# Kernel optimization log

Measured on AMD Instinct MI355X. Metric: run time of the kernel, lower is better.

Reference implementation:

```python
import jax, jax.numpy as jnp
import numpy as np

L_OUT, B, N, C, M, D, T = 4, 4, 1000, 80, 64, 256, 28
CLS_W, L1_W, GIOU_W, MASK_W = 2.0, 5.0, 2.0, 5.0
ALPHA, GAMMA, EPS = 0.25, 2.0, 1e-8
CANDIDATE_K, CENTER_RADIUS, BIG = 10, 2.5, 100000.0


def _areas(b):
    return (b[..., 2] - b[..., 0]) * (b[..., 3] - b[..., 1])


def pairwise_giou(b1, b2):
    # b1 [n,4], b2 [m,4] -> [n,m] generalized IoU (torchvision convention)
    area1, area2 = _areas(b1), _areas(b2)
    lt = jnp.maximum(b1[:, None, :2], b2[None, :, :2])
    rb = jnp.minimum(b1[:, None, 2:], b2[None, :, 2:])
    wh = jnp.clip(rb - lt, 0.0)
    inter = wh[..., 0] * wh[..., 1]
    union = area1[:, None] + area2[None, :] - inter
    iou = inter / union
    lti = jnp.minimum(b1[:, None, :2], b2[None, :, :2])
    rbi = jnp.maximum(b1[:, None, 2:], b2[None, :, 2:])
    whi = jnp.clip(rbi - lti, 0.0)
    areai = whi[..., 0] * whi[..., 1]
    return iou - (areai - union) / areai


def diag_giou(b1, b2):
    # elementwise giou for matched pairs, b1/b2 [n,4] -> [n]
    area1, area2 = _areas(b1), _areas(b2)
    lt = jnp.maximum(b1[:, :2], b2[:, :2])
    rb = jnp.minimum(b1[:, 2:], b2[:, 2:])
    wh = jnp.clip(rb - lt, 0.0)
    inter = wh[:, 0] * wh[:, 1]
    union = area1 + area2 - inter
    iou = inter / union
    lti = jnp.minimum(b1[:, :2], b2[:, :2])
    rbi = jnp.maximum(b1[:, 2:], b2[:, 2:])
    whi = jnp.clip(rbi - lti, 0.0)
    areai = whi[:, 0] * whi[:, 1]
    return iou - (areai - union) / areai


def pairwise_iou(b1, b2, eps=1e-8):
    # mmdet bbox_overlaps, mode='iou'
    area1, area2 = _areas(b1), _areas(b2)
    lt = jnp.maximum(b1[:, None, :2], b2[None, :, :2])
    rb = jnp.minimum(b1[:, None, 2:], b2[None, :, 2:])
    wh = jnp.clip(rb - lt, 0.0)
    inter = wh[..., 0] * wh[..., 1]
    union = jnp.maximum(area1[:, None] + area2[None, :] - inter, eps)
    return inter / union


def simota_match(logits, boxes, gt_cls, gt_boxes, img_size):
    # SimOTA assignment for one image; fixed shapes via masking instead of boolean indexing
    n, c = logits.shape
    m = gt_boxes.shape[0]
    cx = (boxes[:, 0] + boxes[:, 2]) * 0.5
    cy = (boxes[:, 1] + boxes[:, 3]) * 0.5
    w = boxes[:, 2] - boxes[:, 0]
    h = boxes[:, 3] - boxes[:, 1]
    in_gt = ((cx[:, None] > gt_boxes[None, :, 0]) & (cy[:, None] > gt_boxes[None, :, 1])
             & (cx[:, None] < gt_boxes[None, :, 2]) & (cy[:, None] < gt_boxes[None, :, 3]))
    gcx = (gt_boxes[:, 0] + gt_boxes[:, 2]) * 0.5
    gcy = (gt_boxes[:, 1] + gt_boxes[:, 3]) * 0.5
    rx = CENTER_RADIUS * w[:, None]
    ry = CENTER_RADIUS * h[:, None]
    in_ct = ((cx[:, None] > gcx[None, :] - rx) & (cx[:, None] < gcx[None, :] + rx)
             & (cy[:, None] > gcy[None, :] - ry) & (cy[:, None] < gcy[None, :] + ry))
    valid = in_gt.any(1) | in_ct.any(1)
    in_both = in_gt & in_ct
    has_valid = valid.any()
    valid = valid | (~has_valid)          # fallback: all valid when none
    in_both = in_both | (~has_valid)
    # FocalLossCost (mmdet), weight = cls weight
    p = jax.nn.sigmoid(logits)
    neg = -jnp.log(1.0 - p + EPS) * (1.0 - ALPHA) * p ** GAMMA
    pos = -jnp.log(p + EPS) * ALPHA * (1.0 - p) ** GAMMA
    cls_cost = CLS_W * (pos - neg)[:, gt_cls]          # [n,m]
    nb = boxes / img_size
    ngb = gt_boxes / img_size
    l1_cost = L1_W * jnp.abs(nb[:, None, :] - ngb[None, :, :]).sum(-1)
    giou_cost = GIOU_W * (1.0 - pairwise_giou(nb, ngb))
    cost = cls_cost + l1_cost + giou_cost + (~in_both) * BIG
    cost = jnp.where(valid[:, None], cost, 1e15)       # invalid priors never selected
    ious = pairwise_iou(boxes, gt_boxes) * valid[:, None]
    # dynamic_k_matching
    topk_ious, _ = jax.lax.top_k(ious.T, CANDIDATE_K)  # [m,10]
    dyn_k = jnp.maximum(topk_ious.sum(-1).astype(jnp.int32), 1)
    rank = jnp.argsort(jnp.argsort(cost, axis=0), axis=0)
    matching = rank < dyn_k[None, :]                   # [n,m]
    multi = matching.sum(1) > 1
    best = jnp.argmin(cost, axis=1)
    best_oh = best[:, None] == jnp.arange(m)[None, :]
    matching = jnp.where(multi[:, None], best_oh, matching)
    fg = matching.any(1)
    gt_ind = jnp.argmax(matching, axis=1)
    return fg, gt_ind


def per_image_loss(logits, boxes, pfeat, gt_cls, gt_boxes, gt_masks, img_size, w_mask):
    sg = jax.lax.stop_gradient
    fg, gt_ind = simota_match(sg(logits), sg(boxes), gt_cls, sg(gt_boxes), sg(img_size))
    c = logits.shape[1]
    gcls = gt_cls[gt_ind]
    label = jnp.where(fg[:, None], jax.nn.one_hot(gcls, c, dtype=logits.dtype), 0.0)
    # sigmoid focal loss (sum over all n*c logits)
    p = jax.nn.sigmoid(logits)
    ce = -(label * jax.nn.log_sigmoid(logits) + (1.0 - label) * jax.nn.log_sigmoid(-logits))
    p_t = p * label + (1.0 - p) * (1.0 - label)
    alpha_t = ALPHA * label + (1.0 - ALPHA) * (1.0 - label)
    cls_loss = (alpha_t * ce * (1.0 - p_t) ** GAMMA).sum()
    fgf = fg.astype(logits.dtype)
    nb = boxes / img_size
    gb = gt_boxes[gt_ind] / img_size
    l1_loss = (jnp.abs(nb - gb).sum(-1) * fgf).sum()
    giou_loss = ((1.0 - diag_giou(nb, gb)) * fgf).sum()
    # mask head: per-class mask logits from proposal feats; gather only assigned class
    d = pfeat.shape[1]
    tt = T * T
    w_sel = w_mask.reshape(d, c, tt)[:, gcls, :]        # [d,n,tt]
    m_sel = jax.nn.sigmoid(jnp.einsum('nd,dnt->nt', pfeat, w_sel))
    gm = gt_masks.reshape(gt_masks.shape[0], -1)[gt_ind]  # [n,tt]
    inter = (m_sel * gm).sum(-1)
    union = m_sel.sum(-1) + gm.sum(-1) + 1e-8
    mask_loss = ((1.0 - 2.0 * inter / union) * fgf).sum()
    return cls_loss, l1_loss, giou_loss, mask_loss, fgf.sum()


def _forward(pred_logits, pred_boxes, proposal_feat, gt_boxes, gt_masks, image_size, w_mask, gt_classes):
    per = jax.vmap(per_image_loss, in_axes=(0, 0, 0, 0, 0, 0, 0, None))
    total = jnp.zeros(4, dtype=pred_logits.dtype)
    n_out = pred_logits.shape[0]
    for l in range(n_out):   # small fixed loop over output heads
        cl, l1, gl, ml, k = per(pred_logits[l], pred_boxes[l], proposal_feat[l],
                                gt_classes, gt_boxes, gt_masks, image_size, w_mask)
        num_ins = k.sum()
        total = total + jnp.stack([cl.sum(), l1.sum(), gl.sum(), ml.sum()]) / num_ins
    weights = jnp.array([CLS_W, L1_W, GIOU_W, MASK_W], dtype=total.dtype)
    return weights * total / n_out   # [cls, l1, giou, mask] losses


def setup_inputs():
    key = jax.random.key(0)
    ks = jax.random.split(key, 8)

    def rand_boxes(k, shape):
        k1, k2 = jax.random.split(k)
        ctr = jax.random.uniform(k1, shape + (2,), minval=100.0, maxval=700.0)
        wh = jax.random.uniform(k2, shape + (2,), minval=20.0, maxval=300.0)
        return jnp.concatenate([ctr - wh * 0.5, ctr + wh * 0.5], axis=-1)

    pred_logits = jax.random.normal(ks[0], (L_OUT, B, N, C), dtype=jnp.float32)
    pred_boxes = rand_boxes(ks[1], (L_OUT, B, N))
    proposal_feat = 0.1 * jax.random.normal(ks[2], (L_OUT, B, N, D), dtype=jnp.float32)
    gt_boxes = rand_boxes(ks[3], (B, M))
    gt_masks = (jax.random.uniform(ks[4], (B, M, T, T)) > 0.5).astype(jnp.float32)
    image_size = 800.0 * jnp.ones((B,), dtype=jnp.float32)
    w_mask = 0.02 * jax.random.normal(ks[5], (D, C * T * T), dtype=jnp.float32)
    gt_classes = jax.random.randint(ks[6], (B, M), 0, C)
    return {"pred_logits": pred_logits, "pred_boxes": pred_boxes, "proposal_feat": proposal_feat,
            "gt_boxes": gt_boxes, "gt_masks": gt_masks, "image_size": image_size,
            "w_mask": w_mask, "gt_classes": gt_classes}


def reference(pred_logits, pred_boxes, proposal_feat, gt_boxes, gt_masks, image_size, w_mask, gt_classes):
    return _forward(pred_logits, pred_boxes, proposal_feat, gt_boxes, gt_masks, image_size, w_mask, gt_classes)
```

## Files before the change

### kernel.cpp

```cpp
#include <hip/hip_runtime.h>
#include <math.h>
#include <float.h>

#define LOUT 4
#define BATCH 4
#define NP 1000
#define NC 80
#define NM 64
#define ND 256
#define TT 784
#define NIMG (LOUT*BATCH)
#define CWTT (NC*TT)
#define MAXF (NIMG*NP)
#define CH 16
#define TPT 112
#define MAXCH 768

__device__ __forceinline__ float block_reduce_sum(float v, float* red) {
    int tid = threadIdx.x;
    red[tid] = v; __syncthreads();
    for (int s = blockDim.x >> 1; s > 0; s >>= 1) {
        if (tid < s) red[tid] += red[tid + s];
        __syncthreads();
    }
    float r = red[0]; __syncthreads();
    return r;
}

__global__ void __launch_bounds__(256) k_prep(
        const float* __restrict__ logits, const float* __restrict__ boxes,
        const float* __restrict__ gtb, const float* __restrict__ gtm,
        int* __restrict__ valid, unsigned long long* __restrict__ inboth,
        int* __restrict__ hasvalid, float* __restrict__ logT,
        float* __restrict__ negsum, float* __restrict__ gmsum) {
    int blk = blockIdx.x;
    int tid = threadIdx.x;
    __shared__ float red[256];
    __shared__ float tile[32][33];
    if (blk < 256) {
        int bj = blk;
        float s = 0.f;
        for (int t = tid; t < TT; t += 256) s += gtm[(size_t)bj * TT + t];
        float r = block_reduce_sum(s, red);
        if (tid == 0) gmsum[bj] = r;
    } else if (blk < 320) {
        int rel = blk - 256;
        int img = rel >> 2, q = rel & 3, b = img % BATCH;
        float* g = red;
        g[tid] = gtb[b * NM * 4 + tid];
        __syncthreads();
        int i = q * 256 + tid;
        if (i >= NP) return;
        float4 bx = *(const float4*)&boxes[((size_t)img * NP + i) * 4];
        float x0 = bx.x, y0 = bx.y, x1 = bx.z, y1 = bx.w;
        float cx = (x0 + x1) * 0.5f, cy = (y0 + y1) * 0.5f;
        float w = x1 - x0, h = y1 - y0;
        float rx = 2.5f * w, ry = 2.5f * h;
        bool any_gt = false, any_ct = false;
        unsigned long long ib = 0ull;
        for (int j = 0; j < NM; ++j) {
            float gx0 = g[j*4], gy0 = g[j*4+1], gx1 = g[j*4+2], gy1 = g[j*4+3];
            bool igt = (cx > gx0) && (cy > gy0) && (cx < gx1) && (cy < gy1);
            float gcx = (gx0 + gx1) * 0.5f, gcy = (gy0 + gy1) * 0.5f;
            bool ict = (cx > gcx - rx) && (cx < gcx + rx) && (cy > gcy - ry) && (cy < gcy + ry);
            any_gt |= igt; any_ct |= ict;
            if (igt && ict) ib |= (1ull << j);
        }
        bool v = any_gt || any_ct;
        valid[img * NP + i] = v ? 1 : 0;
        inboth[img * NP + i] = ib;
        if (v) atomicOr(&hasvalid[img], 1);
    } else if (blk < 1856) {
        int rel = blk - 320;
        int img = rel / 96; int r2 = rel % 96;
        int i0 = (r2 / 3) * 32, c0 = (r2 % 3) * 32;
        int tx = tid & 31, ty4 = tid >> 5;
        #pragma unroll
        for (int r = 0; r < 4; ++r) {
            int ty = ty4 + r * 8;
            int i = i0 + ty, c = c0 + tx;
            tile[ty][tx] = (i < NP && c < NC) ? logits[((size_t)img * NP + i) * NC + c] : 0.f;
        }
        __syncthreads();
        #pragma unroll
        for (int r = 0; r < 4; ++r) {
            int ty = ty4 + r * 8;
            int c = c0 + ty, i = i0 + tx;
            if (c < NC && i < NP) logT[((size_t)img * NC + c) * NP + i] = tile[tx][ty];
        }
    } else {
        int rel = blk - 1856;
        int img = rel >> 2, q = rel & 3;
        int i = q * 256 + tid;
        if (i >= NP) return;
        const float* lr = logits + ((size_t)img * NP + i) * NC;
        float s = 0.f;
        #pragma unroll 4
        for (int c = 0; c < NC; ++c) {
            float x = lr[c];
            float p = 1.f / (1.f + expf(-x));
            float ax = fabsf(x);
            float sp = log1pf(expf(-ax));
            float ls_neg = fminf(-x, 0.f) - sp;
            s += 0.75f * (-ls_neg) * p * p;
        }
        negsum[img * NP + i] = s;
    }
}

__global__ void __launch_bounds__(256) k_costtopk(
        const float* __restrict__ logT, const float* __restrict__ boxes,
        const float* __restrict__ gtb, const int* __restrict__ gcls_all,
        const float* __restrict__ imsz,
        const int* __restrict__ valid, const unsigned long long* __restrict__ inboth,
        const int* __restrict__ hasvalid,
        float* __restrict__ cost, float* __restrict__ kthc, int* __restrict__ kthi) {
    int img = blockIdx.y, b = img % BATCH;
    int tid = threadIdx.x;
    int w = tid >> 6, l = tid & 63;
    int j = blockIdx.x * 4 + w;
    float s = imsz[b], inv_s = 1.f / s;
    const float* gj = gtb + (b * NM + j) * 4;
    float gx0 = gj[0], gy0 = gj[1], gx1 = gj[2], gy1 = gj[3];
    int gc = gcls_all[b * NM + j];
    int hv = hasvalid[img];
    float garea = (gx1 - gx0) * (gy1 - gy0);
    float ngx0 = gx0 * inv_s, ngy0 = gy0 * inv_s, ngx1 = gx1 * inv_s, ngy1 = gy1 * inv_s;
    float ngarea = (ngx1 - ngx0) * (ngy1 - ngy0);
    size_t colbase = ((size_t)img * NM + j) * NP;
    const float* lrow = logT + ((size_t)img * NC + gc) * NP;
    float icv[16], ccv[16];
    #pragma unroll
    for (int e = 0; e < 16; ++e) {
        int i = e * 64 + l;
        if (i < NP) {
            float4 bx = *(const float4*)&boxes[((size_t)img * NP + i) * 4];
            float x0 = bx.x, y0 = bx.y, x1 = bx.z, y1 = bx.w;
            float area = (x1 - x0) * (y1 - y0);
            float ltx = fmaxf(x0, gx0), lty = fmaxf(y0, gy0);
            float rbx = fminf(x1, gx1), rby = fminf(y1, gy1);
            float iw = fmaxf(rbx - ltx, 0.f), ih = fmaxf(rby - lty, 0.f);
            float inter = iw * ih;
            float uni = fmaxf(area + garea - inter, 1e-8f);
            float iou = inter / uni;
            float nx0 = x0 * inv_s, ny0 = y0 * inv_s, nx1 = x1 * inv_s, ny1 = y1 * inv_s;
            float narea = (nx1 - nx0) * (ny1 - ny0);
            float nltx = fmaxf(nx0, ngx0), nlty = fmaxf(ny0, ngy0);
            float nrbx = fminf(nx1, ngx1), nrby = fminf(ny1, ngy1);
            float niw = fmaxf(nrbx - nltx, 0.f), nih = fmaxf(nrby - nlty, 0.f);
            float ninter = niw * nih;
            float nuni = narea + ngarea - ninter;
            float niou = ninter / nuni;
            float ex0 = fminf(nx0, ngx0), ey0 = fminf(ny0, ngy0);
            float ex1 = fmaxf(nx1, ngx1), ey1 = fmaxf(ny1, ngy1);
            float earea = fmaxf(ex1 - ex0, 0.f) * fmaxf(ey1 - ey0, 0.f);
            float giou = niou - (earea - nuni) / earea;
            float giou_cost = 2.f * (1.f - giou);
            float l1 = 5.f * (fabsf(nx0 - ngx0) + fabsf(ny0 - ngy0) + fabsf(nx1 - ngx1) + fabsf(ny1 - ngy1));
            float x = lrow[i];
            float p = 1.f / (1.f + expf(-x));
            float neg = -logf(1.f - p + 1e-8f) * 0.75f * p * p;
            float pos = -logf(p + 1e-8f) * 0.25f * (1.f - p) * (1.f - p);
            float cls = 2.f * (pos - neg);
            bool vld = (valid[img * NP + i] != 0) || (hv == 0);
            bool inb = (((inboth[img * NP + i] >> j) & 1ull) != 0ull) || (hv == 0);
            float cst = cls + l1 + giou_cost + (inb ? 0.f : 100000.f);
            if (!vld) cst = 1e15f;
            cost[colbase + i] = cst;
            ccv[e] = cst;
            icv[e] = vld ? iou : 0.f;
        } else {
            ccv[e] = FLT_MAX;
            icv[e] = -FLT_MAX;
        }
    }
    unsigned cons = 0;
    float ssum = 0.f;
    for (int it = 0; it < 10; ++it) {
        float bv = -FLT_MAX; int bi = 0x7fffffff;
        #pragma unroll
        for (int e = 0; e < 16; ++e) {
            if (cons & (1u << e)) continue;
            float v = icv[e]; int i = e * 64 + l;
            if ((v > bv) || (v == bv && i < bi)) { bv = v; bi = i; }
        }
        #pragma unroll
        for (int sft = 1; sft < 64; sft <<= 1) {
            float ov = __shfl_xor(bv, sft, 64);
            int oi = __shfl_xor(bi, sft, 64);
            if ((ov > bv) || (ov == bv && oi < bi)) { bv = ov; bi = oi; }
        }
        ssum += bv;
        if ((bi & 63) == l) cons |= 1u << (bi >> 6);
    }
    int dk = (int)ssum; if (dk < 1) dk = 1;
    cons = 0;
    float gv = 0.f; int gi = 0;
    for (int it = 0; it < dk; ++it) {
        float bv = FLT_MAX; int bi = 0x7fffffff;
        #pragma unroll
        for (int e = 0; e < 16; ++e) {
            if (cons & (1u << e)) continue;
            float v = ccv[e]; int i = e * 64 + l;
            if ((v < bv) || (v == bv && i < bi)) { bv = v; bi = i; }
        }
        #pragma unroll
        for (int sft = 1; sft < 64; sft <<= 1) {
            float ov = __shfl_xor(bv, sft, 64);
            int oi = __shfl_xor(bi, sft, 64);
            if ((ov < bv) || (ov == bv && oi < bi)) { bv = ov; bi = oi; }
        }
        if ((bi & 63) == l) cons |= 1u << (bi >> 6);
        gv = bv; gi = bi;
    }
    if (l == 0) { kthc[img * NM + j] = gv; kthi[img * NM + j] = gi; }
}

__global__ void k_match(const float* __restrict__ cost,
                        const float* __restrict__ kthc, const int* __restrict__ kthi,
                        const float* __restrict__ boxes, const float* __restrict__ gtb,
                        const float* __restrict__ imsz, const int* __restrict__ gcls_all,
                        const float* __restrict__ negsum, const float* __restrict__ logT,
                        int* __restrict__ fg, int* __restrict__ gt_ind,
                        int* __restrict__ cnt, float* __restrict__ accum) {
    int img = blockIdx.y, b = img % BATCH;
    int i = blockIdx.x * blockDim.x + threadIdx.x;
    __shared__ float skc[NM]; __shared__ int ski[NM];
    __shared__ float red[256];
    if (threadIdx.x < NM) {
        skc[threadIdx.x] = kthc[img * NM + threadIdx.x];
        ski[threadIdx.x] = kthi[img * NM + threadIdx.x];
    }
    __syncthreads();
    float l1 = 0.f, gl = 0.f, f = 0.f, vcls = 0.f;
    if (i < NP) {
        vcls = negsum[img * NP + i];
        int cntm = 0, first = -1;
        float bc = FLT_MAX; int bj = 0;
        for (int j = 0; j < NM; ++j) {
            float c = cost[((size_t)img * NM + j) * NP + i];
            bool m = (c < skc[j]) || (c == skc[j] && i <= ski[j]);
            if (m) { cntm++; if (first < 0) first = j; }
            if (c < bc) { bc = c; bj = j; }
        }
        int gi = 0, isfg = 0;
        if (cntm > 1) { gi = bj; isfg = 1; }
        else if (cntm == 1) { gi = first; isfg = 1; }
        fg[img * NP + i] = isfg;
        gt_ind[img * NP + i] = gi;
        if (isfg) {
            int gc = gcls_all[b * NM + gi];
            atomicAdd(&cnt[gc], 1);
            float x = logT[((size_t)img * NC + gc) * NP + i];
            float p = 1.f / (1.f + expf(-x));
            float ax = fabsf(x);
            float sp = log1pf(expf(-ax));
            float ls_pos = fminf(x, 0.f) - sp;
            float ls_neg = fminf(-x, 0.f) - sp;
            float pos = 0.25f * (-ls_pos) * (1.f - p) * (1.f - p);
            float neg = 0.75f * (-ls_neg) * p * p;
            vcls += pos - neg;
            float inv = 1.f / imsz[b];
            float4 bx = *(const float4*)&boxes[((size_t)img * NP + i) * 4];
            const float* gj = gtb + (b * NM + gi) * 4;
            float nx0 = bx.x*inv, ny0 = bx.y*inv, nx1 = bx.z*inv, ny1 = bx.w*inv;
            float gx0 = gj[0]*inv, gy0 = gj[1]*inv, gx1 = gj[2]*inv, gy1 = gj[3]*inv;
            l1 = fabsf(nx0-gx0) + fabsf(ny0-gy0) + fabsf(nx1-gx1) + fabsf(ny1-gy1);
            float a1 = (nx1-nx0)*(ny1-ny0), a2 = (gx1-gx0)*(gy1-gy0);
            float ltx = fmaxf(nx0,gx0), lty = fmaxf(ny0,gy0);
            float rbx = fminf(nx1,gx1), rby = fminf(ny1,gy1);
            float iw = fmaxf(rbx-ltx,0.f), ih = fmaxf(rby-lty,0.f);
            float inter = iw*ih, uni = a1+a2-inter, iou = inter/uni;
            float ex0 = fminf(nx0,gx0), ey0 = fminf(ny0,gy0);
            float ex1 = fmaxf(nx1,gx1), ey1 = fmaxf(ny1,gy1);
            float ea = fmaxf(ex1-ex0,0.f)*fmaxf(ey1-ey0,0.f);
            float giou = iou - (ea-uni)/ea;
            gl = 1.f - giou;
            f = 1.f;
        }
    }
    float scl = block_reduce_sum(vcls, red);
    float sl1 = block_reduce_sum(l1, red);
    float sgl = block_reduce_sum(gl, red);
    float sf  = block_reduce_sum(f, red);
    if (threadIdx.x == 0) {
        atomicAdd(&accum[img*5+0], scl);
        atomicAdd(&accum[img*5+1], sl1);
        atomicAdd(&accum[img*5+2], sgl);
        atomicAdd(&accum[img*5+4], sf);
    }
}

__global__ void __launch_bounds__(1024) k_scanscatter(
        const int* __restrict__ cnt, const int* __restrict__ fg,
        const int* __restrict__ gti, const int* __restrict__ gcls,
        int* __restrict__ offs_g, int* __restrict__ total,
        int* __restrict__ chtab, int* __restrict__ nch, int* __restrict__ list) {
    __shared__ int offs[NC]; __shared__ int choff[NC]; __shared__ int sfill[NC];
    int tid = threadIdx.x;
    if (tid == 0) {
        int s = 0, m = 0;
        for (int c = 0; c < NC; ++c) {
            offs[c] = s; s += cnt[c];
            choff[c] = m; m += (cnt[c] + CH - 1) / CH;
        }
        *total = s; *nch = m;
    }
    if (tid < NC) sfill[tid] = 0;
    __syncthreads();
    if (tid < NC) {
        offs_g[tid] = offs[tid];
        int n = cnt[tid], co = choff[tid];
        for (int k = 0; k * CH < n; ++k) chtab[co + k] = (tid << 16) | k;
    }
    for (int idx = tid; idx < NIMG * NP; idx += 1024) {
        if (fg[idx]) {
            int img = idx / NP, i = idx % NP, b = img % BATCH;
            int gt = gti[idx];
            int c = gcls[b * NM + gt];
            int pos = offs[c] + atomicAdd(&sfill[c], 1);
            list[pos] = (img << 16) | (gt << 10) | i;
        }
    }
}

__global__ void __launch_bounds__(128) k_mgemm(
        const float* __restrict__ pfeat, const float* __restrict__ wmask,
        const float* __restrict__ gtm, const int* __restrict__ list,
        const int* __restrict__ cnt, const int* __restrict__ offs,
        const int* __restrict__ chtab, const int* __restrict__ nch,
        float* __restrict__ inter, float* __restrict__ msum) {
    int ch = blockIdx.x;
    if (ch >= *nch) return;
    int e = chtab[ch];
    int c = e >> 16, k = e & 0xffff;
    int base = offs[c] + k * CH;
    int P = min(CH, cnt[c] - k * CH);
    int tid = threadIdx.x;
    bool act = (tid < TPT);
    int t = blockIdx.y * TPT + (act ? tid : 0);
    __shared__ float pf[CH][ND];
    __shared__ int sl[CH];
    if (tid < CH) sl[tid] = (tid < P) ? list[base + tid] : 0;
    __syncthreads();
    for (int idx = tid; idx < CH * (ND / 4); idx += 128) {
        int p = idx >> 6, d4 = idx & 63;
        float4 v = {0.f, 0.f, 0.f, 0.f};
        if (p < P) {
            int pk = sl[p];
            int img = pk >> 16, i = pk & 1023;
            v = *(const float4*)&pfeat[((size_t)img * NP + i) * ND + d4 * 4];
        }
        *(float4*)&pf[p][d4 * 4] = v;
    }
    __syncthreads();
    float acc[CH];
    #pragma unroll
    for (int p = 0; p < CH; ++p) acc[p] = 0.f;
    if (act) {
        const float* wr = wmask + (size_t)c * TT + t;
        float4 wq[4];
        #pragma unroll
        for (int q = 0; q < 4; ++q) {
            const float* wp = wr + (size_t)q * 4 * CWTT;
            wq[q].x = wp[0]; wq[q].y = wp[CWTT];
            wq[q].z = wp[2 * (size_t)CWTT]; wq[q].w = wp[3 * (size_t)CWTT];
        }
        #pragma unroll 4
        for (int d4 = 0; d4 < 60; ++d4) {
            float4 w = wq[d4 & 3];
            const float* wp = wr + (size_t)(d4 + 4) * 4 * CWTT;
            wq[d4 & 3].x = wp[0]; wq[d4 & 3].y = wp[CWTT];
            wq[d4 & 3].z = wp[2 * (size_t)CWTT]; wq[d4 & 3].w = wp[3 * (size_t)CWTT];
            int d = d4 * 4;
            #pragma unroll
            for (int p = 0; p < CH; ++p) {
                float4 q4 = *(const float4*)&pf[p][d];
                acc[p] += q4.x * w.x + q4.y * w.y + q4.z * w.z + q4.w * w.w;
            }
        }
        #pragma unroll
        for (int d4 = 60; d4 < 64; ++d4) {
            float4 w = wq[d4 & 3];
            int d = d4 * 4;
            #pragma unroll
            for (int p = 0; p < CH; ++p) {
                float4 q4 = *(const float4*)&pf[p][d];
                acc[p] += q4.x * w.x + q4.y * w.y + q4.z * w.z + q4.w * w.w;
            }
        }
    }
    #pragma unroll 4
    for (int p = 0; p < CH; ++p) {
        if (p >= P) break;
        int pk = sl[p];
        int img = pk >> 16, j = (pk >> 10) & 63, b = img % BATCH;
        float li = 0.f, lm = 0.f;
        if (act) {
            float m = 1.f / (1.f + expf(-acc[p]));
            float g = gtm[((size_t)(b * NM + j)) * TT + t];
            li = m * g; lm = m;
        }
        #pragma unroll
        for (int s = 32; s > 0; s >>= 1) {
            li += __shfl_down(li, s, 64);
            lm += __shfl_down(lm, s, 64);
        }
        if ((tid & 63) == 0) {
            atomicAdd(&inter[base + p], li);
            atomicAdd(&msum[base + p], lm);
        }
    }
}

__global__ void __launch_bounds__(256) k_dicefinal(
        const int* __restrict__ list, const int* __restrict__ total,
        const float* __restrict__ inter, const float* __restrict__ msum,
        const float* __restrict__ gmsum, const float* __restrict__ accum,
        float* __restrict__ out) {
    __shared__ float md[NIMG];
    int tid = threadIdx.x;
    if (tid < NIMG) md[tid] = 0.f;
    __syncthreads();
    int n = *total;
    for (int e = tid; e < n; e += 256) {
        int pk = list[e];
        int img = pk >> 16, j = (pk >> 10) & 63, b = img % BATCH;
        float d = 1.f - 2.f * inter[e] / (msum[e] + gmsum[b * NM + j] + 1e-8f);
        atomicAdd(&md[img], d);
    }
    __syncthreads();
    if (tid == 0) {
        float tot[4] = {0.f, 0.f, 0.f, 0.f};
        for (int l = 0; l < LOUT; ++l) {
            float s0 = 0.f, s1 = 0.f, s2 = 0.f, s3 = 0.f, s4 = 0.f;
            for (int b = 0; b < BATCH; ++b) {
                int img = l * BATCH + b;
                s0 += accum[img*5+0]; s1 += accum[img*5+1]; s2 += accum[img*5+2];
                s3 += md[img];        s4 += accum[img*5+4];
            }
            tot[0] += s0 / s4; tot[1] += s1 / s4; tot[2] += s2 / s4; tot[3] += s3 / s4;
        }
        const float w[4] = {2.f, 5.f, 2.f, 5.f};
        for (int k = 0; k < 4; ++k) out[k] = w[k] * tot[k] / (float)LOUT;
    }
}

extern "C" void kernel_launch(void* const* d_in, const int* in_sizes, int n_in,
                              void* d_out, int out_size, void* d_ws, size_t ws_size,
                              hipStream_t stream) {
    const float* logits = (const float*)d_in[0];
    const float* boxes  = (const float*)d_in[1];
    const float* pfeat  = (const float*)d_in[2];
    const float* gtb    = (const float*)d_in[3];
    const float* gtm    = (const float*)d_in[4];
    const float* imsz   = (const float*)d_in[5];
    const float* wmask  = (const float*)d_in[6];
    const int*   gcls   = (const int*)d_in[7];

    char* ws = (char*)d_ws;
    size_t off = 0;
    auto alloc = [&](size_t bytes) -> void* {
        void* p = ws + off;
        off = (off + bytes + 255) & ~(size_t)255;
        return p;
    };
    char* zbase = ws;
    float* accum = (float*)alloc(NIMG * 5 * sizeof(float));
    int* cnt    = (int*)alloc(NC * sizeof(int));
    int* hasvalid = (int*)alloc(NIMG * sizeof(int));
    float* interA = (float*)alloc((size_t)MAXF * sizeof(float));
    float* msumA  = (float*)alloc((size_t)MAXF * sizeof(float));
    size_t zbytes = off;
    float* cost = (float*)alloc((size_t)NIMG * NM * NP * sizeof(float));
    float* logT = (float*)alloc((size_t)NIMG * NC * NP * sizeof(float));
    float* negsum = (float*)alloc((size_t)NIMG * NP * sizeof(float));
    int* valid  = (int*)alloc((size_t)NIMG * NP * sizeof(int));
    unsigned long long* inboth = (unsigned long long*)alloc((size_t)NIMG * NP * sizeof(unsigned long long));
    float* kthc = (float*)alloc(NIMG * NM * sizeof(float));
    int* kthi   = (int*)alloc(NIMG * NM * sizeof(int));
    int* fg     = (int*)alloc((size_t)NIMG * NP * sizeof(int));
    int* gti    = (int*)alloc((size_t)NIMG * NP * sizeof(int));
    float* gmsum = (float*)alloc(BATCH * NM * sizeof(float));
    int* offs   = (int*)alloc(NC * sizeof(int));
    int* total  = (int*)alloc(sizeof(int));
    int* nch    = (int*)alloc(sizeof(int));
    int* chtab  = (int*)alloc((size_t)MAXCH * sizeof(int));
    int* list   = (int*)alloc((size_t)MAXF * sizeof(int));

    hipMemsetAsync(zbase, 0, zbytes, stream);

    k_prep<<<1920, 256, 0, stream>>>(logits, boxes, gtb, gtm, valid, inboth, hasvalid, logT, negsum, gmsum);
    k_costtopk<<<dim3(NM / 4, NIMG), 256, 0, stream>>>(logT, boxes, gtb, gcls, imsz, valid, inboth, hasvalid, cost, kthc, kthi);
    k_match<<<dim3((NP + 255) / 256, NIMG), 256, 0, stream>>>(cost, kthc, kthi, boxes, gtb, imsz, gcls, negsum, logT, fg, gti, cnt, accum);
    k_scanscatter<<<1, 1024, 0, stream>>>(cnt, fg, gti, gcls, offs, total, chtab, nch, list);
    k_mgemm<<<dim3(MAXCH, 7), 128, 0, stream>>>(pfeat, wmask, gtm, list, cnt, offs, chtab, nch, interA, msumA);
    k_dicefinal<<<1, 256, 0, stream>>>(list, total, interA, msumA, gmsum, accum, (float*)d_out);
}
```

Baseline: 200.7 us.

## Stream mask weights via async global-to-LDS ring buffer and fold zeroing into prep

The mask GEMM now loads w_mask rows through global_load_lds into an 8-stage shared-memory ring, with explicit vmcnt waits. This replaces the 4-deep register prefetch and is meant to keep more loads in flight and hide global latency. Separately, most of the workspace memset is moved into extra blocks of the prep kernel, leaving only a small memset for hasvalid. The hand-written waitcnt and barrier logic is fragile: the loop does not sync between waves before stage slots are reused, and the global-to-LDS path uses wave-wide per-lane addressing.

Result: slower. 238.6 us (+18.9%).

```diff
diff --git a/kernel.cpp b/kernel.cpp
--- a/kernel.cpp
+++ b/kernel.cpp
@@ -32,7 +32,9 @@
         const float* __restrict__ gtb, const float* __restrict__ gtm,
         int* __restrict__ valid, unsigned long long* __restrict__ inboth,
         int* __restrict__ hasvalid, float* __restrict__ logT,
-        float* __restrict__ negsum, float* __restrict__ gmsum) {
+        float* __restrict__ negsum, float* __restrict__ gmsum,
+        float* __restrict__ interA, float* __restrict__ msumA,
+        float* __restrict__ accum, int* __restrict__ cnt) {
     int blk = blockIdx.x;
     int tid = threadIdx.x;
     __shared__ float red[256];
@@ -88,7 +90,7 @@
             int c = c0 + ty, i = i0 + tx;
             if (c < NC && i < NP) logT[((size_t)img * NC + c) * NP + i] = tile[tx][ty];
         }
-    } else {
+    } else if (blk < 1920) {
         int rel = blk - 1856;
         int img = rel >> 2, q = rel & 3;
         int i = q * 256 + tid;
@@ -105,6 +107,13 @@
             s += 0.75f * (-ls_neg) * p * p;
         }
         negsum[img * NP + i] = s;
+    } else if (blk < 2045) {
+        int idx = (blk - 1920) * 256 + tid;
+        if (idx < 16000) interA[idx] = 0.f;
+        else if (idx < 32000) msumA[idx - 16000] = 0.f;
+    } else {
+        if (tid < 80) accum[tid] = 0.f;
+        else if (tid < 160) cnt[tid - 80] = 0;
     }
 }
 
@@ -324,6 +333,12 @@
     }
 }
 
+__device__ __forceinline__ void gl_lds4(const float* g, float* l) {
+    __builtin_amdgcn_global_load_lds((const __attribute__((address_space(1))) void*)g,
+                                     (__attribute__((address_space(3))) void*)l, 4, 0, 0);
+}
+#define WAITV(N) asm volatile("s_waitcnt vmcnt(" #N ")" ::: "memory")
+
 __global__ void __launch_bounds__(128) k_mgemm(
         const float* __restrict__ pfeat, const float* __restrict__ wmask,
         const float* __restrict__ gtm, const int* __restrict__ list,
@@ -337,9 +352,11 @@
     int base = offs[c] + k * CH;
     int P = min(CH, cnt[c] - k * CH);
     int tid = threadIdx.x;
+    int wave = tid >> 6;
     bool act = (tid < TPT);
     int t = blockIdx.y * TPT + (act ? tid : 0);
     __shared__ float pf[CH][ND];
+    __shared__ float wbuf[8][4][TPT];
     __shared__ int sl[CH];
     if (tid < CH) sl[tid] = (tid < P) ? list[base + tid] : 0;
     __syncthreads();
@@ -353,43 +370,53 @@
         }
         *(float4*)&pf[p][d4 * 4] = v;
     }
-    __syncthreads();
+    const float* wsrc = wmask + (size_t)c * TT + t;
+    int wbase = wave << 6;
+    #define ISSUE(g) do { \
+        if (act) { \
+            const float* gs_ = wsrc + (size_t)((g) * 4) * CWTT; \
+            int s_ = (g) & 7; \
+            gl_lds4(gs_,                       &wbuf[s_][0][wbase]); \
+            gl_lds4(gs_ + CWTT,                &wbuf[s_][1][wbase]); \
+            gl_lds4(gs_ + 2 * (size_t)CWTT,    &wbuf[s_][2][wbase]); \
+            gl_lds4(gs_ + 3 * (size_t)CWTT,    &wbuf[s_][3][wbase]); \
+        } \
+    } while (0)
+    ISSUE(0); ISSUE(1); ISSUE(2); ISSUE(3);
+    ISSUE(4); ISSUE(5); ISSUE(6); ISSUE(7);
+    asm volatile("s_waitcnt lgkmcnt(0)" ::: "memory");
+    __builtin_amdgcn_s_barrier();
     float acc[CH];
     #pragma unroll
     for (int p = 0; p < CH; ++p) acc[p] = 0.f;
-    if (act) {
-        const float* wr = wmask + (size_t)c * TT + t;
-        float4 wq[4];
-        #pragma unroll
-        for (int q = 0; q < 4; ++q) {
-            const float* wp = wr + (size_t)q * 4 * CWTT;
-            wq[q].x = wp[0]; wq[q].y = wp[CWTT];
-            wq[q].z = wp[2 * (size_t)CWTT]; wq[q].w = wp[3 * (size_t)CWTT];
-        }
-        #pragma unroll 4
-        for (int d4 = 0; d4 < 60; ++d4) {
-            float4 w = wq[d4 & 3];
-            const float* wp = wr + (size_t)(d4 + 4) * 4 * CWTT;
-            wq[d4 & 3].x = wp[0]; wq[d4 & 3].y = wp[CWTT];
-            wq[d4 & 3].z = wp[2 * (size_t)CWTT]; wq[d4 & 3].w = wp[3 * (size_t)CWTT];
-            int d = d4 * 4;
-            #pragma unroll
-            for (int p = 0; p < CH; ++p) {
-                float4 q4 = *(const float4*)&pf[p][d];
-                acc[p] += q4.x * w.x + q4.y * w.y + q4.z * w.z + q4.w * w.w;
-            }
-        }
-        #pragma unroll
-        for (int d4 = 60; d4 < 64; ++d4) {
-            float4 w = wq[d4 & 3];
-            int d = d4 * 4;
-            #pragma unroll
-            for (int p = 0; p < CH; ++p) {
-                float4 q4 = *(const float4*)&pf[p][d];
-                acc[p] += q4.x * w.x + q4.y * w.y + q4.z * w.z + q4.w * w.w;
-            }
-        }
-    }
+    #define CONSUME(g) do { \
+        if (act) { \
+            int s_ = (g) & 7; \
+            float w0 = wbuf[s_][0][tid], w1 = wbuf[s_][1][tid]; \
+            float w2 = wbuf[s_][2][tid], w3 = wbuf[s_][3][tid]; \
+            int d_ = (g) * 4; \
+            _Pragma("unroll") \
+            for (int p = 0; p < CH; ++p) { \
+                float4 q4 = *(const float4*)&pf[p][d_]; \
+                acc[p] += q4.x * w0 + q4.y * w1 + q4.z * w2 + q4.w * w3; \
+            } \
+        } \
+    } while (0)
+    for (int g = 0; g < 56; ++g) {
+        WAITV(28);
+        CONSUME(g);
+        ISSUE(g + 8);
+    }
+    WAITV(28); CONSUME(56);
+    WAITV(24); CONSUME(57);
+    WAITV(20); CONSUME(58);
+    WAITV(16); CONSUME(59);
+    WAITV(12); CONSUME(60);
+    WAITV(8);  CONSUME(61);
+    WAITV(4);  CONSUME(62);
+    WAITV(0);  CONSUME(63);
+    #undef ISSUE
+    #undef CONSUME
     #pragma unroll 4
     for (int p = 0; p < CH; ++p) {
         if (p >= P) break;
@@ -465,13 +492,11 @@
         off = (off + bytes + 255) & ~(size_t)255;
         return p;
     };
-    char* zbase = ws;
+    int* hasvalid = (int*)alloc(NIMG * sizeof(int));
     float* accum = (float*)alloc(NIMG * 5 * sizeof(float));
     int* cnt    = (int*)alloc(NC * sizeof(int));
-    int* hasvalid = (int*)alloc(NIMG * sizeof(int));
     float* interA = (float*)alloc((size_t)MAXF * sizeof(float));
     float* msumA  = (float*)alloc((size_t)MAXF * sizeof(float));
-    size_t zbytes = off;
     float* cost = (float*)alloc((size_t)NIMG * NM * NP * sizeof(float));
     float* logT = (float*)alloc((size_t)NIMG * NC * NP * sizeof(float));
     float* negsum = (float*)alloc((size_t)NIMG * NP * sizeof(float));
@@ -488,9 +513,10 @@
     int* chtab  = (int*)alloc((size_t)MAXCH * sizeof(int));
     int* list   = (int*)alloc((size_t)MAXF * sizeof(int));
 
-    hipMemsetAsync(zbase, 0, zbytes, stream);
-
-    k_prep<<<1920, 256, 0, stream>>>(logits, boxes, gtb, gtm, valid, inboth, hasvalid, logT, negsum, gmsum);
+    hipMemsetAsync(hasvalid, 0, NIMG * sizeof(int), stream);
+
+    k_prep<<<2046, 256, 0, stream>>>(logits, boxes, gtb, gtm, valid, inboth, hasvalid,
+                                     logT, negsum, gmsum, interA, msumA, accum, cnt);
     k_costtopk<<<dim3(NM / 4, NIMG), 256, 0, stream>>>(logT, boxes, gtb, gcls, imsz, valid, inboth, hasvalid, cost, kthc, kthi);
     k_match<<<dim3((NP + 255) / 256, NIMG), 256, 0, stream>>>(cost, kthc, kthi, boxes, gtb, imsz, gcls, negsum, logT, fg, gti, cnt, accum);
     k_scanscatter<<<1, 1024, 0, stream>>>(cnt, fg, gti, gcls, offs, total, chtab, nch, list);
```
